# Performance work log

Hardware: AMD Instinct MI355X
Metric: run time of the kernel (lower is better)

Reference implementation:

```python
import jax, jax.numpy as jnp
import numpy as np

V, E, H, L = 10000, 256, 512, 2
B, T, S = 64, 64, 128
NEG = -1e6


def setup_inputs() -> dict:
    key = jax.random.key(0)
    ks = jax.random.split(key, 20)
    sc = 0.02
    inp = {
        "x": jax.random.randint(ks[0], (B, T), 0, V),
        "enc_outputs": jax.random.normal(ks[1], (B, S, H), jnp.float32),
        "h0": jax.random.normal(ks[2], (L, B, H), jnp.float32),
        "valid_lens": jax.random.randint(ks[3], (B,), 1, S + 1).astype(jnp.int32),
        # params
        "emb": jax.random.normal(ks[4], (V, E), jnp.float32) * sc,
        "Wq": jax.random.normal(ks[5], (H, H), jnp.float32) * sc,
        "Wk": jax.random.normal(ks[6], (H, H), jnp.float32) * sc,
        "wv": jax.random.normal(ks[7], (H,), jnp.float32) * sc,
        "W_ih0": jax.random.normal(ks[8], (3 * H, H + E), jnp.float32) * sc,
        "W_hh0": jax.random.normal(ks[9], (3 * H, H), jnp.float32) * sc,
        "b_ih0": jnp.zeros((3 * H,), jnp.float32),
        "b_hh0": jnp.zeros((3 * H,), jnp.float32),
        "W_ih1": jax.random.normal(ks[10], (3 * H, H), jnp.float32) * sc,
        "W_hh1": jax.random.normal(ks[11], (3 * H, H), jnp.float32) * sc,
        "b_ih1": jnp.zeros((3 * H,), jnp.float32),
        "b_hh1": jnp.zeros((3 * H,), jnp.float32),
        "Wd": jax.random.normal(ks[12], (V, H), jnp.float32) * sc,
        "bd": jnp.zeros((V,), jnp.float32),
    }
    return inp


def _gru_cell(x, h, W_ih, W_hh, b_ih, b_hh):
    # PyTorch GRU cell math
    gi = x @ W_ih.T + b_ih  # (B, 3H)
    gh = h @ W_hh.T + b_hh
    ir, iz, in_ = jnp.split(gi, 3, axis=-1)
    hr, hz, hn = jnp.split(gh, 3, axis=-1)
    r = jax.nn.sigmoid(ir + hr)
    z = jax.nn.sigmoid(iz + hz)
    n = jnp.tanh(in_ + r * hn)
    return (1.0 - z) * n + z * h


def reference(x, enc_outputs, h0, valid_lens, emb, Wq, Wk, wv,
              W_ih0, W_hh0, b_ih0, b_hh0, W_ih1, W_hh1, b_ih1, b_hh1, Wd, bd):
    X = emb[x]                     # (B, T, E)
    Xt = jnp.transpose(X, (1, 0, 2))  # (T, B, E) time-major
    k_proj = jnp.einsum('bsh,oh->bso', enc_outputs, Wk)  # precompute W_k(keys)
    mask = jnp.arange(S)[None, :] < valid_lens[:, None]  # (B, S)

    def step(h, x_t):
        q = h[-1]                                      # (B, H) last-layer hidden
        q_proj = q @ Wq.T                              # (B, H)
        feats = jnp.tanh(q_proj[:, None, :] + k_proj)  # (B, S, H)
        scores = jnp.einsum('bsh,h->bs', feats, wv)
        scores = jnp.where(mask, scores, NEG)
        attn = jax.nn.softmax(scores, axis=-1)
        context = jnp.einsum('bs,bsh->bh', attn, enc_outputs)
        inp = jnp.concatenate([context, x_t], axis=-1)  # (B, H+E)
        h0n = _gru_cell(inp, h[0], W_ih0, W_hh0, b_ih0, b_hh0)
        h1n = _gru_cell(h0n, h[1], W_ih1, W_hh1, b_ih1, b_hh1)
        hn = jnp.stack([h0n, h1n])
        return hn, h1n

    _, ys = jax.lax.scan(step, h0, Xt)       # ys: (T, B, H)
    logits = jnp.einsum('tbh,vh->tbv', ys, Wd) + bd
    return jnp.transpose(logits, (1, 0, 2))  # (B, T, V)
```

## Files before the change

kernel.cpp:

```cpp
#include <hip/hip_runtime.h>
#include <hip/hip_bf16.h>

#define Bd 64
#define Td 64
#define Sd 128
#define Hd 512
#define Ed 256
#define Vd 10000
#define NBLK 256

#define W0IH 0
#define W0HH 4608
#define W1IH 7680
#define W1HH 10752
#define WTOT 13824

typedef __attribute__((ext_vector_type(8))) short bf16x8;
typedef __attribute__((ext_vector_type(4))) float f32x4;

__device__ __forceinline__ float fast_tanh(float x) {
  float e = __expf(-2.0f * fabsf(x));
  float r = (1.0f - e) / (1.0f + e);
  return copysignf(r, x);
}
__device__ __forceinline__ float fast_sigmoid(float x) {
  return 1.0f / (1.0f + __expf(-x));
}
__device__ __forceinline__ float bf2f(unsigned short u) {
  return __uint_as_float(((unsigned int)u) << 16);
}
__device__ __forceinline__ void st_llc(float* p, float v) {
  __hip_atomic_store(p, v, __ATOMIC_RELAXED, __HIP_MEMORY_SCOPE_AGENT);
}
__device__ __forceinline__ int q4(int k, int b) {
  return (k >> 2) * 256 + b * 4 + (k & 3);
}

__device__ __forceinline__ void gbar(int* arrive, int* go, int ep, int blk, int tid) {
  __syncthreads();
  if (tid == 0)
    __hip_atomic_store(&arrive[blk], ep, __ATOMIC_RELAXED, __HIP_MEMORY_SCOPE_AGENT);
  if (blk == 0) {
    if (tid < 64) {
      for (;;) {
        int a0 = __hip_atomic_load(&arrive[tid], __ATOMIC_RELAXED,
                                   __HIP_MEMORY_SCOPE_AGENT);
        int a1 = __hip_atomic_load(&arrive[tid + 64], __ATOMIC_RELAXED,
                                   __HIP_MEMORY_SCOPE_AGENT);
        int a2 = __hip_atomic_load(&arrive[tid + 128], __ATOMIC_RELAXED,
                                   __HIP_MEMORY_SCOPE_AGENT);
        int a3 = __hip_atomic_load(&arrive[tid + 192], __ATOMIC_RELAXED,
                                   __HIP_MEMORY_SCOPE_AGENT);
        if (a0 >= ep && a1 >= ep && a2 >= ep && a3 >= ep) break;
        __builtin_amdgcn_s_sleep(2);
      }
    }
    __syncthreads();
    if (tid == 0)
      __hip_atomic_store(go, ep, __ATOMIC_RELAXED, __HIP_MEMORY_SCOPE_AGENT);
  }
  if (tid == 0) {
    while (__hip_atomic_load(go, __ATOMIC_RELAXED, __HIP_MEMORY_SCOPE_AGENT) < ep) {
      __builtin_amdgcn_s_sleep(1);
    }
    __builtin_amdgcn_fence(__ATOMIC_ACQUIRE, "agent");
  }
  __syncthreads();
}

__global__ void k_gemm_kp(const float* __restrict__ A, const float* __restrict__ W,
                          unsigned short* __restrict__ C, int M, int N, int K) {
  __shared__ __align__(16) float As[16][64];
  __shared__ __align__(16) float Ws[16][64];
  int m0 = blockIdx.x * 64, n0 = blockIdx.y * 64;
  int tid = threadIdx.x;
  int tx = tid & 15, ty = tid >> 4;
  float acc[4][4] = {};
  for (int k0 = 0; k0 < K; k0 += 16) {
#pragma unroll
    for (int i = 0; i < 4; i++) {
      int e = tid + i * 256;
      int r = e >> 4, c = e & 15;
      As[c][r] = A[(long)(m0 + r) * K + k0 + c];
      Ws[c][r] = W[(long)(n0 + r) * K + k0 + c];
    }
    __syncthreads();
#pragma unroll
    for (int k = 0; k < 16; k++) {
      float a_[4], w_[4];
#pragma unroll
      for (int i = 0; i < 4; i++) a_[i] = As[k][ty * 4 + i];
#pragma unroll
      for (int j = 0; j < 4; j++) w_[j] = Ws[k][tx * 4 + j];
#pragma unroll
      for (int i = 0; i < 4; i++)
#pragma unroll
        for (int j = 0; j < 4; j++) acc[i][j] += a_[i] * w_[j];
    }
    __syncthreads();
  }
#pragma unroll
  for (int i = 0; i < 4; i++)
#pragma unroll
    for (int j = 0; j < 4; j++) {
      __hip_bfloat16 h = __float2bfloat16(acc[i][j]);
      C[(long)(m0 + ty * 4 + i) * N + n0 + tx * 4 + j] = *(unsigned short*)&h;
    }
}

__global__ __launch_bounds__(256) void k_logits(
    const unsigned short* __restrict__ ysbf, const unsigned short* __restrict__ Wdbf,
    const float* __restrict__ bd, float* __restrict__ out, int N) {
  int m0 = blockIdx.x * 64, n0 = blockIdx.y * 64;
  int w = threadIdx.x >> 6, lane = threadIdx.x & 63;
  int row = lane & 15, kg = lane >> 4;
  int mw = m0 + w * 16;
  f32x4 acc[4] = {};
  const unsigned short* Arow = ysbf + (size_t)(mw + row) * 512 + kg * 8;
  for (int k0 = 0; k0 < 512; k0 += 32) {
    bf16x8 af = *(const bf16x8*)(Arow + k0);
#pragma unroll
    for (int nn = 0; nn < 4; nn++) {
      int ncol = n0 + nn * 16 + row;
      bf16x8 bfv = {};
      if (ncol < N) bfv = *(const bf16x8*)(Wdbf + (size_t)ncol * 512 + k0 + kg * 8);
      acc[nn] = __builtin_amdgcn_mfma_f32_16x16x32_bf16(af, bfv, acc[nn], 0, 0, 0);
    }
  }
#pragma unroll
  for (int nn = 0; nn < 4; nn++) {
    int ncol = n0 + nn * 16 + row;
    if (ncol < N) {
      float bv = bd[ncol];
#pragma unroll
      for (int r = 0; r < 4; r++) {
        int mm = mw + kg * 4 + r;
        int t_ = mm >> 6, b_ = mm & 63;
        out[((size_t)(b_ * Td + t_)) * N + ncol] = acc[nn][r] + bv;
      }
    }
  }
}

__global__ void k_tobf(const float* __restrict__ src, unsigned short* __restrict__ dst,
                       long n) {
  long i = (long)blockIdx.x * 1024 + threadIdx.x;
  if (i < n) {
    __hip_bfloat16 h = __float2bfloat16(src[i]);
    dst[i] = *(unsigned short*)&h;
  }
}

__global__ void k_wqT(const float* __restrict__ Wq, unsigned short* __restrict__ WqT) {
  __shared__ float tile[64][65];
  int bi = blockIdx.x, bj = blockIdx.y;
  int tx = threadIdx.x & 63, ty = threadIdx.x >> 6;
  for (int i = 0; i < 64; i += 4)
    tile[ty + i][tx] = Wq[(size_t)(bi * 64 + ty + i) * 512 + bj * 64 + tx];
  __syncthreads();
  for (int i = 0; i < 64; i += 4) {
    int r = ty + i;
    __hip_bfloat16 h = __float2bfloat16(tile[tx][r]);
    WqT[(size_t)(bj * 64 + r) * 512 + bi * 64 + tx] = *(unsigned short*)&h;
  }
}

__global__ void k_embT(const int* __restrict__ x, const float* __restrict__ emb,
                       float* __restrict__ embTf) {
  __shared__ int rows[64];
  int t = blockIdx.x;
  if (threadIdx.x < 64) rows[threadIdx.x] = x[threadIdx.x * Td + t];
  __syncthreads();
  int e = threadIdx.x;
  for (int b = 0; b < 64; b++) {
    embTf[(size_t)t * 16384 + q4(e, b)] = emb[(long)rows[b] * Ed + e];
  }
}

template <bool C0>
__device__ __forceinline__ void cell_phase(
    int blk, int tid, int t, const float* __restrict__ aT,
    const float* __restrict__ embTf, const float* __restrict__ hT,
    const float* wIH, const float* wHH, const float* __restrict__ bih,
    const float* __restrict__ bhh, const float* __restrict__ den,
    float* __restrict__ houtT, unsigned short* __restrict__ ysbf, float* scratch) {
  int lane = tid & 63;
  int w = tid >> 6;
  const int RIH = C0 ? 768 : 512;
  float* ps = scratch;
  float* psE = scratch + 3072;
  if (w < 8) {
    int strm = w >> 2, qk = w & 3;
    const float* A = (strm == 0 ? aT : hT) + qk * 32 * 256;
    float a[6] = {0.f, 0.f, 0.f, 0.f, 0.f, 0.f};
#pragma unroll 8
    for (int k4 = 0; k4 < 32; k4++) {
      float4 av = *(const float4*)&A[k4 * 256 + lane * 4];
#pragma unroll
      for (int r = 0; r < 6; r++) {
        const float* wr = (strm == 0 ? wIH + (size_t)r * RIH : wHH + (size_t)r * 512) +
                          qk * 128 + k4 * 4;
        float4 w4 = *(const float4*)wr;
        a[r] += av.x * w4.x + av.y * w4.y + av.z * w4.z + av.w * w4.w;
      }
    }
    int base = strm * 6;
#pragma unroll
    for (int r = 0; r < 6; r++) ps[((base + r) * 4 + qk) * 64 + lane] = a[r];
  } else if (C0 && w < 12) {
    int qe = w - 8;
    const float* ef = embTf + (size_t)t * 16384 + qe * 16 * 256;
    float a[6] = {0.f, 0.f, 0.f, 0.f, 0.f, 0.f};
#pragma unroll 8
    for (int k4 = 0; k4 < 16; k4++) {
      float4 ev = *(const float4*)&ef[k4 * 256 + lane * 4];
#pragma unroll
      for (int r = 0; r < 6; r++) {
        const float* wr = wIH + (size_t)r * 768 + 512 + qe * 64 + k4 * 4;
        float4 w4 = *(const float4*)wr;
        a[r] += ev.x * w4.x + ev.y * w4.y + ev.z * w4.z + ev.w * w4.w;
      }
    }
#pragma unroll
    for (int r = 0; r < 6; r++) psE[(r * 4 + qe) * 64 + lane] = a[r];
  }
  __syncthreads();
  if (tid < 128) {
    int jl = tid >> 6, b = tid & 63;
    float invd = C0 ? (1.0f / den[b]) : 1.0f;
#define RD(R)                                                              \
  (ps[((R)*4 + 0) * 64 + b] + ps[((R)*4 + 1) * 64 + b] +                   \
   ps[((R)*4 + 2) * 64 + b] + ps[((R)*4 + 3) * 64 + b])
#define RE(R)                                                              \
  (psE[((R)*4 + 0) * 64 + b] + psE[((R)*4 + 1) * 64 + b] +                 \
   psE[((R)*4 + 2) * 64 + b] + psE[((R)*4 + 3) * 64 + b])
    float ir = RD(0 + jl);
    float iz = RD(2 + jl);
    float in = RD(4 + jl);
    if (C0) {
      ir = ir * invd + RE(0 + jl);
      iz = iz * invd + RE(2 + jl);
      in = in * invd + RE(4 + jl);
    }
    float hr = RD(6 + jl);
    float hz = RD(8 + jl);
    float hn_ = RD(10 + jl);
#undef RD
#undef RE
    int j = blk * 2 + jl;
    float r = fast_sigmoid(ir + hr + bih[j] + bhh[j]);
    float z = fast_sigmoid(iz + hz + bih[Hd + j] + bhh[Hd + j]);
    float n = fast_tanh(in + bih[2 * Hd + j] + r * (hn_ + bhh[2 * Hd + j]));
    float hp = hT[q4(j, b)];
    float out = (1.f - z) * n + z * hp;
    st_llc(&houtT[q4(j, b)], out);
    if (!C0) {
      __hip_bfloat16 hb = __float2bfloat16(out);
      ysbf[((size_t)t * 64 + b) * 512 + j] = *(unsigned short*)&hb;
    }
  }
}

__global__ __launch_bounds__(1024, 1) void k_decoder(
    const float* __restrict__ h0_in, const int* __restrict__ vlen,
    const unsigned short* __restrict__ WqTbf, const float* __restrict__ wvp,
    const float* __restrict__ Wih0, const float* __restrict__ Whh0,
    const float* __restrict__ bih0, const float* __restrict__ bhh0,
    const float* __restrict__ Wih1, const float* __restrict__ Whh1,
    const float* __restrict__ bih1, const float* __restrict__ bhh1,
    const unsigned short* __restrict__ kpbf, const unsigned short* __restrict__ encbf,
    const float* __restrict__ embTf, int* bar, float* ctxT, float* den,
    float* h0TA, float* h0TB, float* h1TA, float* h1TB, unsigned short* ysbf) {
  __shared__ __align__(16) float wLDS[WTOT];
  __shared__ __align__(16) unsigned short kpL[32 * 512];
  __shared__ __align__(16) unsigned short encL[32 * 512];
  __shared__ __align__(16) float scratch[4608];
  __shared__ __align__(16) float h1s[512];
  int blk = blockIdx.x, tid = threadIdx.x;
  int lane = tid & 63;
  int w = tid >> 6;
  int battn = blk >> 2, q = blk & 3;
  int* arrive = bar;
  int* go = bar + NBLK;
  int ep = 0;

  {
    int j0 = blk * 2;
#pragma unroll
    for (int rr = 0; rr < 6; rr++) {
      int g = rr >> 1, jl = rr & 1;
      int row = g * Hd + j0 + jl;
      const float* s0 = Wih0 + (size_t)row * 768;
      for (int k = tid; k < 768; k += 1024) wLDS[W0IH + rr * 768 + k] = s0[k];
      const float* s1 = Whh0 + (size_t)row * Hd;
      for (int k = tid; k < Hd; k += 1024) wLDS[W0HH + rr * 512 + k] = s1[k];
      const float* s2 = Wih1 + (size_t)row * Hd;
      for (int k = tid; k < Hd; k += 1024) wLDS[W1IH + rr * 512 + k] = s2[k];
      const float* s3 = Whh1 + (size_t)row * Hd;
      for (int k = tid; k < Hd; k += 1024) wLDS[W1HH + rr * 512 + k] = s3[k];
    }
    const uint4* ksrc = (const uint4*)(kpbf + ((size_t)battn * Sd + q * 32) * Hd);
    const uint4* esrc = (const uint4*)(encbf + ((size_t)battn * Sd + q * 32) * Hd);
    uint4* kdst = (uint4*)kpL;
    uint4* edst = (uint4*)encL;
    for (int i = tid; i < 2048; i += 1024) {
      kdst[i] = ksrc[i];
      edst[i] = esrc[i];
    }
  }
  float wvr[8];
#pragma unroll
  for (int i = 0; i < 8; i++) wvr[i] = wvp[lane * 8 + i];

  if (blk < Bd) {
    int b = blk;
    for (int k = tid; k < Hd; k += 1024) {
      st_llc(&h0TA[q4(k, b)], h0_in[(0 * Bd + b) * Hd + k]);
      st_llc(&h1TA[q4(k, b)], h0_in[(1 * Bd + b) * Hd + k]);
    }
  }
  if (tid < 128) st_llc(&ctxT[blk * 128 + tid], 0.f);
  if (blk < Bd && tid == 128) st_llc(&den[blk], 0.f);
  gbar(arrive, go, ++ep, blk, tid);

  for (int t = 0; t < Td; t++) {
    const float* h0prev = (t & 1) ? h0TB : h0TA;
    float* h0next = (t & 1) ? h0TA : h0TB;
    const float* h1prev = (t & 1) ? h1TB : h1TA;
    float* h1next = (t & 1) ? h1TA : h1TB;

    {
      int b = battn;
      if (tid < 512) h1s[tid] = h1prev[q4(tid, b)];
      __syncthreads();
      float* qpP = scratch;
      float* qpF = scratch + 4096;
      if (w < 8) {
        float p[8] = {0.f, 0.f, 0.f, 0.f, 0.f, 0.f, 0.f, 0.f};
        const unsigned short* Wt = WqTbf + (size_t)(w * 64) * 512 + lane * 8;
#pragma unroll 8
        for (int kk = 0; kk < 64; kk++) {
          float hv = h1s[w * 64 + kk];
          uint4 u = *(const uint4*)(Wt + (size_t)kk * 512);
          p[0] += hv * __uint_as_float(u.x << 16);
          p[1] += hv * __uint_as_float(u.x & 0xffff0000u);
          p[2] += hv * __uint_as_float(u.y << 16);
          p[3] += hv * __uint_as_float(u.y & 0xffff0000u);
          p[4] += hv * __uint_as_float(u.z << 16);
          p[5] += hv * __uint_as_float(u.z & 0xffff0000u);
          p[6] += hv * __uint_as_float(u.w << 16);
          p[7] += hv * __uint_as_float(u.w & 0xffff0000u);
        }
#pragma unroll
        for (int i = 0; i < 8; i++) qpP[w * 512 + lane * 8 + i] = p[i];
      }
      __syncthreads();
      if (tid < 512) {
        float s = 0.f;
#pragma unroll
        for (int ww = 0; ww < 8; ww++) s += qpP[ww * 512 + tid];
        qpF[tid] = s;
      }
      __syncthreads();
      float qv[8];
#pragma unroll
      for (int i = 0; i < 8; i++) qv[i] = qpF[lane * 8 + i];
      float* sc = scratch + 4608 - 640;
      int vl = vlen[b];
#pragma unroll
      for (int si = 0; si < 2; si++) {
        int sl = w * 2 + si;
        uint4 kw = *(const uint4*)&kpL[sl * 512 + lane * 8];
        float f0 = __uint_as_float(kw.x << 16);
        float f1 = __uint_as_float(kw.x & 0xffff0000u);
        float f2 = __uint_as_float(kw.y << 16);
        float f3 = __uint_as_float(kw.y & 0xffff0000u);
        float f4 = __uint_as_float(kw.z << 16);
        float f5 = __uint_as_float(kw.z & 0xffff0000u);
        float f6 = __uint_as_float(kw.w << 16);
        float f7 = __uint_as_float(kw.w & 0xffff0000u);
        float acc = wvr[0] * fast_tanh(qv[0] + f0) + wvr[1] * fast_tanh(qv[1] + f1) +
                    wvr[2] * fast_tanh(qv[2] + f2) + wvr[3] * fast_tanh(qv[3] + f3) +
                    wvr[4] * fast_tanh(qv[4] + f4) + wvr[5] * fast_tanh(qv[5] + f5) +
                    wvr[6] * fast_tanh(qv[6] + f6) + wvr[7] * fast_tanh(qv[7] + f7);
#pragma unroll
        for (int off = 1; off < 64; off <<= 1) acc += __shfl_xor(acc, off);
        if (lane == 0) {
          int s = q * 32 + sl;
          sc[sl] = (s < vl) ? __expf(acc) : 0.f;
        }
      }
      __syncthreads();
      if (tid < 32) {
        float p2 = sc[tid];
#pragma unroll
        for (int off = 1; off < 32; off <<= 1) p2 += __shfl_xor(p2, off, 32);
        if (tid == 0) atomicAdd(&den[b], p2);
      }
      if (tid < 512) {
        float acc = 0.f;
#pragma unroll 8
        for (int s = 0; s < 32; s++) acc += sc[s] * bf2f(encL[s * 512 + tid]);
        atomicAdd(&ctxT[q4(tid, b)], acc);
      }
    }
    gbar(arrive, go, ++ep, blk, tid);

    cell_phase<true>(blk, tid, t, ctxT, embTf, h0prev, wLDS + W0IH, wLDS + W0HH,
                     bih0, bhh0, den, h0next, nullptr, scratch);
    gbar(arrive, go, ++ep, blk, tid);

    if (tid < 128) st_llc(&ctxT[blk * 128 + tid], 0.f);
    if (blk < Bd && tid == 128) st_llc(&den[blk], 0.f);
    cell_phase<false>(blk, tid, t, h0next, nullptr, h1prev, wLDS + W1IH,
                      wLDS + W1HH, bih1, bhh1, nullptr, h1next, ysbf, scratch);
    gbar(arrive, go, ++ep, blk, tid);
  }
}

extern "C" void kernel_launch(void* const* d_in, const int* in_sizes, int n_in,
                              void* d_out, int out_size, void* d_ws, size_t ws_size,
                              hipStream_t stream) {
  const int* x = (const int*)d_in[0];
  const float* enc = (const float*)d_in[1];
  const float* h0 = (const float*)d_in[2];
  const int* vlen = (const int*)d_in[3];
  const float* emb = (const float*)d_in[4];
  const float* Wq = (const float*)d_in[5];
  const float* Wk = (const float*)d_in[6];
  const float* wv = (const float*)d_in[7];
  const float* W_ih0 = (const float*)d_in[8];
  const float* W_hh0 = (const float*)d_in[9];
  const float* b_ih0 = (const float*)d_in[10];
  const float* b_hh0 = (const float*)d_in[11];
  const float* W_ih1 = (const float*)d_in[12];
  const float* W_hh1 = (const float*)d_in[13];
  const float* b_ih1 = (const float*)d_in[14];
  const float* b_hh1 = (const float*)d_in[15];
  const float* Wd = (const float*)d_in[16];
  const float* bd = (const float*)d_in[17];
  float* out = (float*)d_out;

  char* p = (char*)d_ws;
  int* bar = (int*)p;
  p += 2048;
  unsigned short* kpbf = (unsigned short*)p;
  p += (size_t)Bd * Sd * Hd * 2;
  unsigned short* encbf = (unsigned short*)p;
  p += (size_t)Bd * Sd * Hd * 2;
  unsigned short* Wdbf = (unsigned short*)p;
  p += (size_t)Vd * Hd * 2;
  unsigned short* WqTbf = (unsigned short*)p;
  p += (size_t)Hd * Hd * 2;
  unsigned short* ysbf = (unsigned short*)p;
  p += (size_t)Td * Bd * Hd * 2;
  float* embTf = (float*)p;
  p += (size_t)Td * Ed * Bd * 4;
  float* ctxT = (float*)p;  p += (size_t)Hd * Bd * 4;
  float* den = (float*)p;   p += 256;
  float* h0TA = (float*)p;  p += (size_t)Hd * Bd * 4;
  float* h0TB = (float*)p;  p += (size_t)Hd * Bd * 4;
  float* h1TA = (float*)p;  p += (size_t)Hd * Bd * 4;
  float* h1TB = (float*)p;

  hipMemsetAsync(bar, 0, 2048, stream);

  k_gemm_kp<<<dim3(128, 8), 256, 0, stream>>>(enc, Wk, kpbf, Bd * Sd, Hd, Hd);
  long nenc = (long)Bd * Sd * Hd;
  k_tobf<<<(nenc + 1023) / 1024, 1024, 0, stream>>>(enc, encbf, nenc);
  long nwd = (long)Vd * Hd;
  k_tobf<<<(nwd + 1023) / 1024, 1024, 0, stream>>>(Wd, Wdbf, nwd);
  k_wqT<<<dim3(8, 8), 256, 0, stream>>>(Wq, WqTbf);
  k_embT<<<Td, 256, 0, stream>>>(x, emb, embTf);
  k_decoder<<<NBLK, 1024, 0, stream>>>(h0, vlen, WqTbf, wv, W_ih0, W_hh0, b_ih0,
                                       b_hh0, W_ih1, W_hh1, b_ih1, b_hh1, kpbf,
                                       encbf, embTf, bar, ctxT, den, h0TA, h0TB,
                                       h1TA, h1TB, ysbf);
  k_logits<<<dim3(64, 157), 256, 0, stream>>>(ysbf, Wdbf, bd, out, Vd);
}
```

Baseline: 4.500 ms.

## Distribute query projection across blocks with LDS-resident Wq slice and extra grid barrier

Previously each block recomputed the full 512-wide query projection for its batch row, streaming the whole bf16 Wq matrix from global memory every timestep. Now each block keeps two fp32 rows of Wq in LDS, computes those two output features for all 64 batch rows, and writes them to a shared global qpN buffer. An extra grid-wide barrier per timestep makes the results visible before attention reads them. This removes the redundant Wq traffic and the bf16 transpose kernel, at the cost of one more global synchronisation per step.

```diff
diff --git a/kernel.cpp b/kernel.cpp
--- a/kernel.cpp
+++ b/kernel.cpp
@@ -148,20 +148,6 @@
   if (i < n) {
     __hip_bfloat16 h = __float2bfloat16(src[i]);
     dst[i] = *(unsigned short*)&h;
-  }
-}
-
-__global__ void k_wqT(const float* __restrict__ Wq, unsigned short* __restrict__ WqT) {
-  __shared__ float tile[64][65];
-  int bi = blockIdx.x, bj = blockIdx.y;
-  int tx = threadIdx.x & 63, ty = threadIdx.x >> 6;
-  for (int i = 0; i < 64; i += 4)
-    tile[ty + i][tx] = Wq[(size_t)(bi * 64 + ty + i) * 512 + bj * 64 + tx];
-  __syncthreads();
-  for (int i = 0; i < 64; i += 4) {
-    int r = ty + i;
-    __hip_bfloat16 h = __float2bfloat16(tile[tx][r]);
-    WqT[(size_t)(bj * 64 + r) * 512 + bi * 64 + tx] = *(unsigned short*)&h;
   }
 }
 
@@ -263,19 +249,20 @@
 
 __global__ __launch_bounds__(1024, 1) void k_decoder(
     const float* __restrict__ h0_in, const int* __restrict__ vlen,
-    const unsigned short* __restrict__ WqTbf, const float* __restrict__ wvp,
+    const float* __restrict__ Wq, const float* __restrict__ wvp,
     const float* __restrict__ Wih0, const float* __restrict__ Whh0,
     const float* __restrict__ bih0, const float* __restrict__ bhh0,
     const float* __restrict__ Wih1, const float* __restrict__ Whh1,
     const float* __restrict__ bih1, const float* __restrict__ bhh1,
     const unsigned short* __restrict__ kpbf, const unsigned short* __restrict__ encbf,
-    const float* __restrict__ embTf, int* bar, float* ctxT, float* den,
-    float* h0TA, float* h0TB, float* h1TA, float* h1TB, unsigned short* ysbf) {
+    const float* __restrict__ embTf, int* bar, float* qpN, float* ctxT,
+    float* den, float* h0TA, float* h0TB, float* h1TA, float* h1TB,
+    unsigned short* ysbf) {
   __shared__ __align__(16) float wLDS[WTOT];
+  __shared__ __align__(16) float WqL[1024];
   __shared__ __align__(16) unsigned short kpL[32 * 512];
   __shared__ __align__(16) unsigned short encL[32 * 512];
   __shared__ __align__(16) float scratch[4608];
-  __shared__ __align__(16) float h1s[512];
   int blk = blockIdx.x, tid = threadIdx.x;
   int lane = tid & 63;
   int w = tid >> 6;
@@ -299,6 +286,7 @@
       const float* s3 = Whh1 + (size_t)row * Hd;
       for (int k = tid; k < Hd; k += 1024) wLDS[W1HH + rr * 512 + k] = s3[k];
     }
+    WqL[tid] = Wq[(size_t)(blk * 2 + (tid >> 9)) * Hd + (tid & 511)];
     const uint4* ksrc = (const uint4*)(kpbf + ((size_t)battn * Sd + q * 32) * Hd);
     const uint4* esrc = (const uint4*)(encbf + ((size_t)battn * Sd + q * 32) * Hd);
     uint4* kdst = (uint4*)kpL;
@@ -330,42 +318,35 @@
     float* h1next = (t & 1) ? h1TA : h1TB;
 
     {
+      int rl = w >> 3, ks = w & 7;
+      const float* qrow = &WqL[rl * 512 + ks * 64];
+      const float* hp4 = h1prev + (ks * 16) * 256 + lane * 4;
+      float acc = 0.f;
+#pragma unroll
+      for (int kk = 0; kk < 64; kk += 4) {
+        float4 hv = *(const float4*)&hp4[(kk >> 2) * 256];
+        acc += hv.x * qrow[kk] + hv.y * qrow[kk + 1] + hv.z * qrow[kk + 2] +
+               hv.w * qrow[kk + 3];
+      }
+      scratch[w * 64 + lane] = acc;
+      __syncthreads();
+      if (tid < 128) {
+        int rl2 = tid >> 6, b = tid & 63;
+        float s = 0.f;
+#pragma unroll
+        for (int qq = 0; qq < 8; qq++) s += scratch[(rl2 * 8 + qq) * 64 + b];
+        st_llc(&qpN[(size_t)b * 512 + blk * 2 + rl2], s);
+      }
+    }
+    gbar(arrive, go, ++ep, blk, tid);
+
+    {
       int b = battn;
-      if (tid < 512) h1s[tid] = h1prev[q4(tid, b)];
-      __syncthreads();
-      float* qpP = scratch;
-      float* qpF = scratch + 4096;
-      if (w < 8) {
-        float p[8] = {0.f, 0.f, 0.f, 0.f, 0.f, 0.f, 0.f, 0.f};
-        const unsigned short* Wt = WqTbf + (size_t)(w * 64) * 512 + lane * 8;
-#pragma unroll 8
-        for (int kk = 0; kk < 64; kk++) {
-          float hv = h1s[w * 64 + kk];
-          uint4 u = *(const uint4*)(Wt + (size_t)kk * 512);
-          p[0] += hv * __uint_as_float(u.x << 16);
-          p[1] += hv * __uint_as_float(u.x & 0xffff0000u);
-          p[2] += hv * __uint_as_float(u.y << 16);
-          p[3] += hv * __uint_as_float(u.y & 0xffff0000u);
-          p[4] += hv * __uint_as_float(u.z << 16);
-          p[5] += hv * __uint_as_float(u.z & 0xffff0000u);
-          p[6] += hv * __uint_as_float(u.w << 16);
-          p[7] += hv * __uint_as_float(u.w & 0xffff0000u);
-        }
-#pragma unroll
-        for (int i = 0; i < 8; i++) qpP[w * 512 + lane * 8 + i] = p[i];
-      }
-      __syncthreads();
-      if (tid < 512) {
-        float s = 0.f;
-#pragma unroll
-        for (int ww = 0; ww < 8; ww++) s += qpP[ww * 512 + tid];
-        qpF[tid] = s;
-      }
-      __syncthreads();
+      float* sc = scratch;
       float qv[8];
-#pragma unroll
-      for (int i = 0; i < 8; i++) qv[i] = qpF[lane * 8 + i];
-      float* sc = scratch + 4608 - 640;
+      const float* qb = qpN + (size_t)b * 512 + lane * 8;
+#pragma unroll
+      for (int i = 0; i < 8; i++) qv[i] = qb[i];
       int vl = vlen[b];
 #pragma unroll
       for (int si = 0; si < 2; si++) {
@@ -450,12 +431,11 @@
   p += (size_t)Bd * Sd * Hd * 2;
   unsigned short* Wdbf = (unsigned short*)p;
   p += (size_t)Vd * Hd * 2;
-  unsigned short* WqTbf = (unsigned short*)p;
-  p += (size_t)Hd * Hd * 2;
   unsigned short* ysbf = (unsigned short*)p;
   p += (size_t)Td * Bd * Hd * 2;
   float* embTf = (float*)p;
   p += (size_t)Td * Ed * Bd * 4;
+  float* qpN = (float*)p;   p += (size_t)Bd * Hd * 4;
   float* ctxT = (float*)p;  p += (size_t)Hd * Bd * 4;
   float* den = (float*)p;   p += 256;
   float* h0TA = (float*)p;  p += (size_t)Hd * Bd * 4;
@@ -470,11 +450,10 @@
   k_tobf<<<(nenc + 1023) / 1024, 1024, 0, stream>>>(enc, encbf, nenc);
   long nwd = (long)Vd * Hd;
   k_tobf<<<(nwd + 1023) / 1024, 1024, 0, stream>>>(Wd, Wdbf, nwd);
-  k_wqT<<<dim3(8, 8), 256, 0, stream>>>(Wq, WqTbf);
   k_embT<<<Td, 256, 0, stream>>>(x, emb, embTf);
-  k_decoder<<<NBLK, 1024, 0, stream>>>(h0, vlen, WqTbf, wv, W_ih0, W_hh0, b_ih0,
+  k_decoder<<<NBLK, 1024, 0, stream>>>(h0, vlen, Wq, wv, W_ih0, W_hh0, b_ih0,
                                        b_hh0, W_ih1, W_hh1, b_ih1, b_hh1, kpbf,
-                                       encbf, embTf, bar, ctxT, den, h0TA, h0TB,
-                                       h1TA, h1TB, ysbf);
+                                       encbf, embTf, bar, qpN, ctxT, den, h0TA,
+                                       h0TB, h1TA, h1TB, ysbf);
   k_logits<<<dim3(64, 157), 256, 0, stream>>>(ysbf, Wdbf, bd, out, Vd);
 }
```

After: 3.762 ms. -16.4%, faster.
